# Optimization experiments

Measured on AMD Instinct MI355X. Metric: run time of the kernel, lower is better.

Reference implementation:

```python
import jax, jax.numpy as jnp
import numpy as np

D_MODEL = 1024
N_HEAD = 16


def setup_inputs() -> dict:
    key = jax.random.key(0)
    ks = jax.random.split(key, 11)
    B, T, D = 4, 2048, D_MODEL
    s = 1.0 / np.sqrt(D)
    inp = {
        "q": jax.random.normal(ks[0], (B, T, D), jnp.float32),
        "k": jax.random.normal(ks[1], (B, T, D), jnp.float32),
        "v": jax.random.normal(ks[2], (B, T, D), jnp.float32),
        "wq": jax.random.normal(ks[3], (D, D), jnp.float32) * s,
        "bq": jnp.zeros((D,), jnp.float32),
        "wk": jax.random.normal(ks[4], (D, D), jnp.float32) * s,
        "bk": jnp.zeros((D,), jnp.float32),
        "wv": jax.random.normal(ks[5], (D, D), jnp.float32) * s,
        "bv": jnp.zeros((D,), jnp.float32),
        "wo": jax.random.normal(ks[6], (D, D), jnp.float32) * s,
        "bo": jnp.zeros((D,), jnp.float32),
    }
    return inp


def reference(q, k, v, wq, bq, wk, bk, wv, bv, wo, bo):
    B, T, D = q.shape
    H = N_HEAD
    hd = D // H  # head dim
    # torch nn.Linear: y = x @ W.T + b
    qh = (q @ wq.T + bq).reshape(B, T, H, hd).transpose(0, 2, 1, 3)  # [B,H,T,hd]
    kh = (k @ wk.T + bk).reshape(B, T, H, hd).transpose(0, 2, 1, 3)
    vh = (v @ wv.T + bv).reshape(B, T, H, hd).transpose(0, 2, 1, 3)
    scale = 1.0 / jnp.sqrt(jnp.asarray(hd, qh.dtype))
    score = jnp.einsum("bhqd,bhkd->bhqk", qh, kh) * scale  # [B,H,T,T]
    causal = jnp.tril(jnp.ones((T, T), dtype=bool))
    score = jnp.where(causal, score, jnp.asarray(-jnp.inf, score.dtype))
    attn = jax.nn.softmax(score, axis=-1)
    out = jnp.einsum("bhqk,bhkd->bhqd", attn, vh)  # [B,H,T,hd]
    out = out.transpose(0, 2, 1, 3).reshape(B, T, D)
    return out @ wo.T + bo
```

## Files before the change

kernel.cpp:

```cpp
#include <hip/hip_runtime.h>
#include <hip/hip_bf16.h>

#define D_MODEL 1024
#define N_HEAD  16
#define HD      64
#define T_SEQ   2048
#define B_SZ    4
#define M_ROWS  (B_SZ * T_SEQ)

typedef __bf16 bf16;
typedef __bf16 bf16x4 __attribute__((ext_vector_type(4)));
typedef __bf16 bf16x8 __attribute__((ext_vector_type(8)));
typedef float  floatx4 __attribute__((ext_vector_type(4)));

__device__ __forceinline__ floatx4 fzero4() {
    floatx4 z = {0.f, 0.f, 0.f, 0.f};
    return z;
}

__device__ __forceinline__ void async_ld16(const void* g, void* l) {
    __builtin_amdgcn_global_load_lds(
        (const __attribute__((address_space(1))) void*)g,
        (__attribute__((address_space(3))) void*)l,
        16, 0, 0);
}

struct CvtArgs {
    const float* s[7];
    bf16* d[7];
    int n[7];
};

__global__ __launch_bounds__(256) void cvt7_kernel(CvtArgs a)
{
    const float* src = a.s[blockIdx.y];
    bf16* dst = a.d[blockIdx.y];
    int n8 = a.n[blockIdx.y];
    int i = blockIdx.x * blockDim.x + threadIdx.x;
    int stride = gridDim.x * blockDim.x;
    for (; i < n8; i += stride) {
        float4 x = ((const float4*)src)[2 * i];
        float4 y = ((const float4*)src)[2 * i + 1];
        bf16x8 o;
        o[0] = (bf16)x.x; o[1] = (bf16)x.y; o[2] = (bf16)x.z; o[3] = (bf16)x.w;
        o[4] = (bf16)y.x; o[5] = (bf16)y.y; o[6] = (bf16)y.z; o[7] = (bf16)y.w;
        ((bf16x8*)dst)[i] = o;
    }
}

template <int OMODE>
__global__ __launch_bounds__(256) void gemm_bf16(
    const bf16* __restrict__ A0, const bf16* __restrict__ W0,
    const float* __restrict__ b0v, void* __restrict__ O0, float scl0,
    const bf16* __restrict__ A1, const bf16* __restrict__ W1,
    const float* __restrict__ b1v, void* __restrict__ O1, float scl1)
{
    __shared__ bf16 ldsA[128 * 64];
    __shared__ bf16 ldsW[128 * 64];

    const bf16* A     = blockIdx.z ? A1 : A0;
    const bf16* W     = blockIdx.z ? W1 : W0;
    const float* bias = blockIdx.z ? b1v : b0v;
    void* Out         = blockIdx.z ? O1 : O0;
    const float scl   = blockIdx.z ? scl1 : scl0;

    const int tid  = threadIdx.x;
    const int wave = tid >> 6, lane = tid & 63;
    const int quad = lane >> 4, l15 = lane & 15;
    const int wr = wave >> 1, wc = wave & 1;
    const int m0 = blockIdx.y * 128, n0 = blockIdx.x * 128;

    floatx4 acc[4][4];
#pragma unroll
    for (int i = 0; i < 4; ++i)
#pragma unroll
        for (int j = 0; j < 4; ++j) acc[i][j] = fzero4();

    const int ro = lane >> 3;
    const int gc = (lane & 7) ^ ro;
    const bf16* gA = A + (size_t)(m0 + wave * 32 + ro) * 1024 + gc * 8;
    const bf16* gW = W + (size_t)(n0 + wave * 32 + ro) * 1024 + gc * 8;

    for (int kt = 0; kt < 16; ++kt) {
        __syncthreads();
#pragma unroll
        for (int j = 0; j < 4; ++j)
            async_ld16((const void*)(gA + kt * 64 + j * 8 * 1024), &ldsA[(wave * 32 + j * 8) * 64]);
#pragma unroll
        for (int j = 0; j < 4; ++j)
            async_ld16((const void*)(gW + kt * 64 + j * 8 * 1024), &ldsW[(wave * 32 + j * 8) * 64]);
        __syncthreads();

#pragma unroll
        for (int ks = 0; ks < 2; ++ks) {
            const int pos = ((ks * 4 + quad) ^ (l15 & 7)) * 8;
            bf16x8 af[4], bw[4];
#pragma unroll
            for (int i = 0; i < 4; ++i)
                af[i] = *(const bf16x8*)(&ldsA[(wr * 64 + i * 16 + l15) * 64 + pos]);
#pragma unroll
            for (int j = 0; j < 4; ++j)
                bw[j] = *(const bf16x8*)(&ldsW[(wc * 64 + j * 16 + l15) * 64 + pos]);
#pragma unroll
            for (int i = 0; i < 4; ++i)
#pragma unroll
                for (int j = 0; j < 4; ++j)
                    acc[i][j] = __builtin_amdgcn_mfma_f32_16x16x32_bf16(af[i], bw[j], acc[i][j], 0, 0, 0);
        }
    }

#pragma unroll
    for (int i = 0; i < 4; ++i) {
#pragma unroll
        for (int j = 0; j < 4; ++j) {
#pragma unroll
            for (int r = 0; r < 4; ++r) {
                int m = m0 + wr * 64 + i * 16 + quad * 4 + r;
                int n = n0 + wc * 64 + j * 16 + l15;
                float val = (acc[i][j][r] + bias[n]) * scl;
                if (OMODE == 2) {
                    ((float*)Out)[(size_t)m * 1024 + n] = val;
                } else {
                    int b = m >> 11, t = m & 2047;
                    int h = n >> 6,  d = n & 63;
                    size_t addr;
                    if (OMODE == 0)
                        addr = ((size_t)(b * N_HEAD + h) * T_SEQ + t) * HD + d;
                    else
                        addr = ((size_t)(b * N_HEAD + h) * HD + d) * T_SEQ + t;
                    ((bf16*)Out)[addr] = (bf16)val;
                }
            }
        }
    }
}

__global__ __launch_bounds__(256, 3) void attn_kernel(
    const bf16* __restrict__ Qh, const bf16* __restrict__ Kh,
    const bf16* __restrict__ Vt, bf16* __restrict__ AO)
{
    __shared__ bf16 Ks[128 * 64];
    __shared__ bf16 Vts[64 * 128];
    __shared__ bf16 Ps[128 * 72];

    const int tid  = threadIdx.x;
    const int wave = tid >> 6, lane = tid & 63;
    const int quad = lane >> 4, l15 = lane & 15;
    const int bh = blockIdx.y;
    const size_t base = (size_t)bh * T_SEQ * HD;
    const int bb = bh >> 4, hh = bh & 15;

    const int kro = lane >> 3;
    const int kgc = (lane & 7) ^ kro;
    const bf16* kgbase = Kh + base + (size_t)(wave * 32 + kro) * HD + kgc * 8;
    const int vrow_lo = (lane >> 4);
    const int vchunk  = (lane & 15);

    for (int phase = 0; phase < 2; ++phase) {
        const int qt = phase ? blockIdx.x : 15 - blockIdx.x;

        bf16x8 qf[2][2];
        const bf16* qbase = Qh + base + (size_t)(qt * 128 + wave * 32) * HD;
#pragma unroll
        for (int ti = 0; ti < 2; ++ti)
#pragma unroll
            for (int ks = 0; ks < 2; ++ks)
                qf[ti][ks] = *(const bf16x8*)(qbase + (ti * 16 + l15) * HD + ks * 32 + quad * 8);

        float mrow[2] = {-1e30f, -1e30f}, lrow[2] = {0.f, 0.f};
        floatx4 oacc[2][4];
#pragma unroll
        for (int ti = 0; ti < 2; ++ti)
#pragma unroll
            for (int nj = 0; nj < 4; ++nj) oacc[ti][nj] = fzero4();

        for (int kt = 0; kt <= qt; ++kt) {
            __syncthreads();
#pragma unroll
            for (int j = 0; j < 4; ++j)
                async_ld16((const void*)(kgbase + (size_t)(kt * 128 + j * 8) * HD),
                           &Ks[(wave * 32 + j * 8) * 64]);
#pragma unroll
            for (int j = 0; j < 4; ++j) {
                int d = wave * 16 + j * 4 + vrow_lo;
                int gcv = vchunk ^ (d & 15);
                async_ld16((const void*)(Vt + base + (size_t)d * T_SEQ + kt * 128 + gcv * 8),
                           &Vts[(wave * 16 + j * 4) * 128]);
            }
            __syncthreads();

            const bool diag = (kt == qt);
            const int lim = diag ? (2 * wave + 1) : 7;

            floatx4 sacc[2][8];
#pragma unroll
            for (int ti = 0; ti < 2; ++ti)
#pragma unroll
                for (int tj = 0; tj < 8; ++tj) sacc[ti][tj] = fzero4();
#pragma unroll
            for (int ks = 0; ks < 2; ++ks) {
                const int pos = ((ks * 4 + quad) ^ (l15 & 7)) * 8;
#pragma unroll
                for (int tj = 0; tj < 8; ++tj) {
                    if (tj <= lim) {
                        bf16x8 kf = *(const bf16x8*)(&Ks[(tj * 16 + l15) * 64 + pos]);
                        sacc[0][tj] = __builtin_amdgcn_mfma_f32_16x16x32_bf16(kf, qf[0][ks], sacc[0][tj], 0, 0, 0);
                        sacc[1][tj] = __builtin_amdgcn_mfma_f32_16x16x32_bf16(kf, qf[1][ks], sacc[1][tj], 0, 0, 0);
                    }
                }
            }

#pragma unroll
            for (int ti = 0; ti < 2; ++ti) {
                const int ql = wave * 32 + ti * 16 + l15;
                float mx = -1e30f;
#pragma unroll
                for (int tj = 0; tj < 8; ++tj) {
                    if (tj <= lim) {
#pragma unroll
                        for (int r = 0; r < 4; ++r) {
                            float s = sacc[ti][tj][r];
                            if (diag && (tj * 16 + quad * 4 + r) > ql) s = -1e30f;
                            sacc[ti][tj][r] = s;
                            mx = fmaxf(mx, s);
                        }
                    }
                }
                mx = fmaxf(mx, __shfl_xor(mx, 16));
                mx = fmaxf(mx, __shfl_xor(mx, 32));
                float mnew  = fmaxf(mrow[ti], mx);
                float alpha = exp2f(mrow[ti] - mnew);
                float rsum  = 0.f;
#pragma unroll
                for (int tj = 0; tj < 8; ++tj) {
                    if (tj <= lim) {
#pragma unroll
                        for (int r = 0; r < 4; ++r) {
                            float p = exp2f(sacc[ti][tj][r] - mnew);
                            rsum += p;
                            sacc[ti][tj][r] = p;
                        }
                    }
                }
                rsum += __shfl_xor(rsum, 16);
                rsum += __shfl_xor(rsum, 32);
                lrow[ti] = lrow[ti] * alpha + rsum;
                mrow[ti] = mnew;
#pragma unroll
                for (int r = 0; r < 4; ++r) {
                    float ar = __shfl(alpha, quad * 4 + r);
#pragma unroll
                    for (int nj = 0; nj < 4; ++nj)
                        oacc[ti][nj][r] *= ar;
                }
            }

#pragma unroll
            for (int h2 = 0; h2 < 2; ++h2) {
                if (4 * h2 > lim) break;
#pragma unroll
                for (int ti = 0; ti < 2; ++ti) {
                    const int ql = wave * 32 + ti * 16 + l15;
#pragma unroll
                    for (int tjo = 0; tjo < 4; ++tjo) {
                        int tj = 4 * h2 + tjo;
                        if (tj <= lim) {
                            bf16x4 pv;
#pragma unroll
                            for (int r = 0; r < 4; ++r) pv[r] = (bf16)sacc[ti][tj][r];
                            *(bf16x4*)(&Ps[ql * 72 + tjo * 16 + quad * 4]) = pv;
                        }
                    }
                }
#pragma unroll
                for (int ks2 = 0; ks2 < 2; ++ks2) {
                    const int gks = 2 * h2 + ks2;
                    if (diag && gks > wave) break;
                    bf16x8 pf[2];
                    pf[0] = *(const bf16x8*)(&Ps[(wave * 32 + l15) * 72 + ks2 * 32 + quad * 8]);
                    pf[1] = *(const bf16x8*)(&Ps[(wave * 32 + 16 + l15) * 72 + ks2 * 32 + quad * 8]);
#pragma unroll
                    for (int nj = 0; nj < 4; ++nj) {
                        int pos = ((gks * 4 + quad) ^ l15) * 8;
                        bf16x8 vf = *(const bf16x8*)(&Vts[(nj * 16 + l15) * 128 + pos]);
                        oacc[0][nj] = __builtin_amdgcn_mfma_f32_16x16x32_bf16(pf[0], vf, oacc[0][nj], 0, 0, 0);
                        oacc[1][nj] = __builtin_amdgcn_mfma_f32_16x16x32_bf16(pf[1], vf, oacc[1][nj], 0, 0, 0);
                    }
                }
            }
        }

#pragma unroll
        for (int ti = 0; ti < 2; ++ti) {
#pragma unroll
            for (int r = 0; r < 4; ++r) {
                float lv = __shfl(lrow[ti], quad * 4 + r);
                float rl = 1.f / lv;
                int qrow = qt * 128 + wave * 32 + ti * 16 + quad * 4 + r;
#pragma unroll
                for (int nj = 0; nj < 4; ++nj) {
                    int d = nj * 16 + l15;
                    AO[((size_t)(bb * T_SEQ + qrow)) * D_MODEL + hh * HD + d] =
                        (bf16)(oacc[ti][nj][r] * rl);
                }
            }
        }
    }
}

extern "C" void kernel_launch(void* const* d_in, const int* in_sizes, int n_in,
                              void* d_out, int out_size, void* d_ws, size_t ws_size,
                              hipStream_t stream)
{
    const float* q  = (const float*)d_in[0];
    const float* k  = (const float*)d_in[1];
    const float* v  = (const float*)d_in[2];
    const float* wq = (const float*)d_in[3];
    const float* bq = (const float*)d_in[4];
    const float* wk = (const float*)d_in[5];
    const float* bk = (const float*)d_in[6];
    const float* wv = (const float*)d_in[7];
    const float* bv = (const float*)d_in[8];
    const float* wo = (const float*)d_in[9];
    const float* bo = (const float*)d_in[10];

    char* ws  = (char*)d_ws;
    char* dob = (char*)d_out;
    const size_t MB = 1024 * 1024;

    bf16* Wqb = (bf16*)(ws);
    bf16* Wkb = (bf16*)(ws + 2 * MB);
    bf16* Wvb = (bf16*)(ws + 4 * MB);
    bf16* Vb  = (bf16*)(ws + 6 * MB);
    bf16* AO  = (bf16*)(ws + 6 * MB);
    bf16* Qh  = (bf16*)(ws + 22 * MB);
    bf16* Kh  = (bf16*)(ws + 38 * MB);
    bf16* Wob = (bf16*)(ws + 54 * MB);
    bf16* Qb  = (bf16*)(dob);
    bf16* Kb  = (bf16*)(dob + 16 * MB);
    bf16* Vt  = (bf16*)(dob);

    const int NQ8 = M_ROWS * D_MODEL / 8;
    const int NW8 = D_MODEL * D_MODEL / 8;
    const float QSCALE = 0.18033688011112042f;

    CvtArgs ca;
    ca.s[0] = q;  ca.d[0] = Qb;  ca.n[0] = NQ8;
    ca.s[1] = k;  ca.d[1] = Kb;  ca.n[1] = NQ8;
    ca.s[2] = v;  ca.d[2] = Vb;  ca.n[2] = NQ8;
    ca.s[3] = wq; ca.d[3] = Wqb; ca.n[3] = NW8;
    ca.s[4] = wk; ca.d[4] = Wkb; ca.n[4] = NW8;
    ca.s[5] = wv; ca.d[5] = Wvb; ca.n[5] = NW8;
    ca.s[6] = wo; ca.d[6] = Wob; ca.n[6] = NW8;

    hipLaunchKernelGGL(cvt7_kernel, dim3(512, 7), dim3(256), 0, stream, ca);
    hipLaunchKernelGGL((gemm_bf16<0>), dim3(8, 64, 2), dim3(256), 0, stream,
                       Qb, Wqb, bq, (void*)Qh, QSCALE,
                       Kb, Wkb, bk, (void*)Kh, 1.0f);
    hipLaunchKernelGGL((gemm_bf16<1>), dim3(8, 64, 1), dim3(256), 0, stream,
                       Vb, Wvb, bv, (void*)Vt, 1.0f,
                       Vb, Wvb, bv, (void*)Vt, 1.0f);
    hipLaunchKernelGGL(attn_kernel, dim3(8, 64), dim3(256), 0, stream, Qh, Kh, Vt, AO);
    hipLaunchKernelGGL((gemm_bf16<2>), dim3(8, 64, 1), dim3(256), 0, stream,
                       AO, Wob, bo, d_out, 1.0f,
                       AO, Wob, bo, d_out, 1.0f);
}
```

Measured before the change: 376.6 us.

## Register-prefetch K/V tiles, lazy softmax rescale, MFMA priority, split reductions

Replaces async global-to-LDS loads with register prefetch of the next K/V tile, issued after the barrier so the loads overlap the current tile's compute. Adds a lazy online-softmax rescale that skips the output rescale unless the row max grows by more than 8. Raises wave priority around the MFMA blocks and splits the max and sum reductions into independent partials. Launch bounds drop from 3 to 2 blocks per CU to make room for the extra prefetch registers, which costs occupancy.

New measurement: 354.6 us. 5.8% less time.

```diff
diff --git a/kernel.cpp b/kernel.cpp
--- a/kernel.cpp
+++ b/kernel.cpp
@@ -135,7 +135,7 @@
     }
 }
 
-__global__ __launch_bounds__(256, 3) void attn_kernel(
+__global__ __launch_bounds__(256, 2) void attn_kernel(
     const bf16* __restrict__ Qh, const bf16* __restrict__ Kh,
     const bf16* __restrict__ Vt, bf16* __restrict__ AO)
 {
@@ -153,8 +153,20 @@
     const int kro = lane >> 3;
     const int kgc = (lane & 7) ^ kro;
     const bf16* kgbase = Kh + base + (size_t)(wave * 32 + kro) * HD + kgc * 8;
-    const int vrow_lo = (lane >> 4);
-    const int vchunk  = (lane & 15);
+    const int vrow_lo = lane >> 4;
+    const int vchunk  = lane & 15;
+
+    const bf16* vgbase[4];
+    bf16* kdst[4];
+    bf16* vdst[4];
+#pragma unroll
+    for (int j = 0; j < 4; ++j) {
+        int d = wave * 16 + j * 4 + vrow_lo;
+        int gcv = vchunk ^ (d & 15);
+        vgbase[j] = Vt + base + (size_t)d * T_SEQ + gcv * 8;
+        vdst[j]   = &Vts[d * 128 + vchunk * 8];
+        kdst[j]   = &Ks[(wave * 32 + j * 8 + kro) * 64 + (lane & 7) * 8];
+    }
 
     for (int phase = 0; phase < 2; ++phase) {
         const int qt = phase ? blockIdx.x : 15 - blockIdx.x;
@@ -167,6 +179,14 @@
             for (int ks = 0; ks < 2; ++ks)
                 qf[ti][ks] = *(const bf16x8*)(qbase + (ti * 16 + l15) * HD + ks * 32 + quad * 8);
 
+        bf16x8 kreg[4], vreg[4];
+#pragma unroll
+        for (int j = 0; j < 4; ++j)
+            kreg[j] = *(const bf16x8*)(kgbase + (size_t)(j * 8) * HD);
+#pragma unroll
+        for (int j = 0; j < 4; ++j)
+            vreg[j] = *(const bf16x8*)(vgbase[j]);
+
         float mrow[2] = {-1e30f, -1e30f}, lrow[2] = {0.f, 0.f};
         floatx4 oacc[2][4];
 #pragma unroll
@@ -177,17 +197,19 @@
         for (int kt = 0; kt <= qt; ++kt) {
             __syncthreads();
 #pragma unroll
-            for (int j = 0; j < 4; ++j)
-                async_ld16((const void*)(kgbase + (size_t)(kt * 128 + j * 8) * HD),
-                           &Ks[(wave * 32 + j * 8) * 64]);
-#pragma unroll
-            for (int j = 0; j < 4; ++j) {
-                int d = wave * 16 + j * 4 + vrow_lo;
-                int gcv = vchunk ^ (d & 15);
-                async_ld16((const void*)(Vt + base + (size_t)d * T_SEQ + kt * 128 + gcv * 8),
-                           &Vts[(wave * 16 + j * 4) * 128]);
-            }
+            for (int j = 0; j < 4; ++j) *(bf16x8*)kdst[j] = kreg[j];
+#pragma unroll
+            for (int j = 0; j < 4; ++j) *(bf16x8*)vdst[j] = vreg[j];
             __syncthreads();
+
+            if (kt < qt) {
+#pragma unroll
+                for (int j = 0; j < 4; ++j)
+                    kreg[j] = *(const bf16x8*)(kgbase + (size_t)((kt + 1) * 128 + j * 8) * HD);
+#pragma unroll
+                for (int j = 0; j < 4; ++j)
+                    vreg[j] = *(const bf16x8*)(vgbase[j] + (kt + 1) * 128);
+            }
 
             const bool diag = (kt == qt);
             const int lim = diag ? (2 * wave + 1) : 7;
@@ -197,6 +219,7 @@
             for (int ti = 0; ti < 2; ++ti)
 #pragma unroll
                 for (int tj = 0; tj < 8; ++tj) sacc[ti][tj] = fzero4();
+            __builtin_amdgcn_s_setprio(1);
 #pragma unroll
             for (int ks = 0; ks < 2; ++ks) {
                 const int pos = ((ks * 4 + quad) ^ (l15 & 7)) * 8;
@@ -209,11 +232,12 @@
                     }
                 }
             }
+            __builtin_amdgcn_s_setprio(0);
 
 #pragma unroll
             for (int ti = 0; ti < 2; ++ti) {
                 const int ql = wave * 32 + ti * 16 + l15;
-                float mx = -1e30f;
+                float mxp[4] = {-1e30f, -1e30f, -1e30f, -1e30f};
 #pragma unroll
                 for (int tj = 0; tj < 8; ++tj) {
                     if (tj <= lim) {
@@ -222,37 +246,42 @@
                             float s = sacc[ti][tj][r];
                             if (diag && (tj * 16 + quad * 4 + r) > ql) s = -1e30f;
                             sacc[ti][tj][r] = s;
-                            mx = fmaxf(mx, s);
+                            mxp[r] = fmaxf(mxp[r], s);
                         }
                     }
                 }
+                float mx = fmaxf(fmaxf(mxp[0], mxp[1]), fmaxf(mxp[2], mxp[3]));
                 mx = fmaxf(mx, __shfl_xor(mx, 16));
                 mx = fmaxf(mx, __shfl_xor(mx, 32));
-                float mnew  = fmaxf(mrow[ti], mx);
-                float alpha = exp2f(mrow[ti] - mnew);
-                float rsum  = 0.f;
+                if (__any(mx > mrow[ti] + 8.0f)) {
+                    float mnew  = fmaxf(mrow[ti], mx);
+                    float alpha = exp2f(mrow[ti] - mnew);
+                    mrow[ti] = mnew;
+                    lrow[ti] *= alpha;
+#pragma unroll
+                    for (int r = 0; r < 4; ++r) {
+                        float ar = __shfl(alpha, quad * 4 + r);
+#pragma unroll
+                        for (int nj = 0; nj < 4; ++nj)
+                            oacc[ti][nj][r] *= ar;
+                    }
+                }
+                float rs[4] = {0.f, 0.f, 0.f, 0.f};
 #pragma unroll
                 for (int tj = 0; tj < 8; ++tj) {
                     if (tj <= lim) {
 #pragma unroll
                         for (int r = 0; r < 4; ++r) {
-                            float p = exp2f(sacc[ti][tj][r] - mnew);
-                            rsum += p;
+                            float p = exp2f(sacc[ti][tj][r] - mrow[ti]);
+                            rs[r] += p;
                             sacc[ti][tj][r] = p;
                         }
                     }
                 }
+                float rsum = (rs[0] + rs[1]) + (rs[2] + rs[3]);
                 rsum += __shfl_xor(rsum, 16);
                 rsum += __shfl_xor(rsum, 32);
-                lrow[ti] = lrow[ti] * alpha + rsum;
-                mrow[ti] = mnew;
-#pragma unroll
-                for (int r = 0; r < 4; ++r) {
-                    float ar = __shfl(alpha, quad * 4 + r);
-#pragma unroll
-                    for (int nj = 0; nj < 4; ++nj)
-                        oacc[ti][nj][r] *= ar;
-                }
+                lrow[ti] += rsum;
             }
 
 #pragma unroll
@@ -279,6 +308,7 @@
                     bf16x8 pf[2];
                     pf[0] = *(const bf16x8*)(&Ps[(wave * 32 + l15) * 72 + ks2 * 32 + quad * 8]);
                     pf[1] = *(const bf16x8*)(&Ps[(wave * 32 + 16 + l15) * 72 + ks2 * 32 + quad * 8]);
+                    __builtin_amdgcn_s_setprio(1);
 #pragma unroll
                     for (int nj = 0; nj < 4; ++nj) {
                         int pos = ((gks * 4 + quad) ^ l15) * 8;
@@ -286,6 +316,7 @@
                         oacc[0][nj] = __builtin_amdgcn_mfma_f32_16x16x32_bf16(pf[0], vf, oacc[0][nj], 0, 0, 0);
                         oacc[1][nj] = __builtin_amdgcn_mfma_f32_16x16x32_bf16(pf[1], vf, oacc[1][nj], 0, 0, 0);
                     }
+                    __builtin_amdgcn_s_setprio(0);
                 }
             }
         }
```
